# Optimization experiments

Hardware: AMD Instinct MI355X
Metric: run time of the kernel (lower is better)

Reference implementation:

```python
import jax, jax.numpy as jnp
import numpy as np

N_NODES = 50000
N_EDGES = 800000
D_NODE = 64
D_EDGE = 64


def setup_inputs() -> dict:
    key = jax.random.key(0)
    ks = jax.random.split(key, 8)
    s = lambda fan_in: 1.0 / np.sqrt(fan_in)
    return {
        "feats": jax.random.normal(ks[0], (N_NODES, D_NODE), dtype=jnp.float32),
        "edge_index": jax.random.randint(ks[1], (N_EDGES, 2), 0, N_NODES, dtype=jnp.int64),
        "edge_attr": jax.random.normal(ks[2], (N_EDGES, D_EDGE), dtype=jnp.float32),
        "W1e": jax.random.normal(ks[3], (2 * D_NODE + D_EDGE, 64), dtype=jnp.float32) * s(192),
        "b1e": jnp.zeros((64,), dtype=jnp.float32),
        "W2e": jax.random.normal(ks[4], (64, D_EDGE), dtype=jnp.float32) * s(64),
        "b2e": jnp.zeros((D_EDGE,), dtype=jnp.float32),
        "W1n": jax.random.normal(ks[5], (D_NODE + D_EDGE, 64), dtype=jnp.float32) * s(128),
        "b1n": jnp.zeros((64,), dtype=jnp.float32),
        "W2n": jax.random.normal(ks[6], (64, D_NODE), dtype=jnp.float32) * s(64),
        "b2n": jnp.zeros((D_NODE,), dtype=jnp.float32),
    }


def reference(feats, edge_index, edge_attr, W1e, b1e, W2e, b2e, W1n, b1n, W2n, b2n):
    r = edge_index[:, 0]
    c = edge_index[:, 1]
    n_nodes = feats.shape[0]

    # Edge model: gather source/target node feats, concat with edge_attr, MLP.
    x = jnp.concatenate([feats[r], feats[c], edge_attr], axis=1)  # [E, 2*d_node+d_edge]
    e = jax.nn.relu(x @ W1e + b1e) @ W2e + b2e                    # [E, d_edge]

    # Node model: mean-aggregate incoming edge messages by target node, concat, MLP.
    agg = jax.ops.segment_sum(e, c, num_segments=n_nodes)         # [N, d_edge]
    deg = jax.ops.segment_sum(jnp.ones((e.shape[0], 1), e.dtype), c, num_segments=n_nodes)
    agg = agg / jnp.maximum(deg, 1.0)
    h = jnp.concatenate([feats, agg], axis=1)                     # [N, d_node+d_edge]
    feats_out = jax.nn.relu(h @ W1n + b1n) @ W2n + b2n            # [N, d_node]

    return feats_out, e
```

## Files before the change

### kernel.cpp

```cpp
#include <hip/hip_runtime.h>

#define NN 50000
#define NE 800000
#define D 64

typedef float v4f __attribute__((ext_vector_type(4)));
typedef int v2i __attribute__((ext_vector_type(2)));

template <bool NT>
__device__ __forceinline__ void mlp_accum64(const float* __restrict__ x,
                                            const float* __restrict__ W,
                                            float scale, float* h) {
    const v4f* x4 = (const v4f*)x;
    #pragma unroll 1
    for (int k0 = 0; k0 < D; k0 += 8) {
        v4f v0, v1;
        if (NT) {
            v0 = __builtin_nontemporal_load(x4 + k0 / 4);
            v1 = __builtin_nontemporal_load(x4 + k0 / 4 + 1);
        } else {
            v0 = x4[k0 / 4];
            v1 = x4[k0 / 4 + 1];
        }
        float xa[8];
        xa[0] = v0[0]; xa[1] = v0[1]; xa[2] = v0[2]; xa[3] = v0[3];
        xa[4] = v1[0]; xa[5] = v1[1]; xa[6] = v1[2]; xa[7] = v1[3];
        #pragma unroll
        for (int kk = 0; kk < 8; ++kk) {
            const float xk = xa[kk] * scale;
            const float* Wr = W + (k0 + kk) * D;
            #pragma unroll
            for (int j = 0; j < D; ++j) h[j] = fmaf(xk, Wr[j], h[j]);
        }
    }
}

__device__ __forceinline__ void mlp_layer2(const float* __restrict__ W2,
                                           const float* __restrict__ b2,
                                           const float* h, float* acc,
                                           float* myrow) {
    #pragma unroll
    for (int j = 0; j < D; ++j) acc[j] = b2[j];
    #pragma unroll
    for (int half = 0; half < 2; ++half) {
        #pragma unroll
        for (int k = 0; k < 32; ++k) myrow[k] = fmaxf(h[half * 32 + k], 0.f);
        #pragma unroll 1
        for (int k = 0; k < 32; ++k) {
            const float hk = myrow[k];
            const float* Wr = W2 + (half * 32 + k) * D;
            #pragma unroll
            for (int j = 0; j < D; ++j) acc[j] = fmaf(hk, Wr[j], acc[j]);
        }
    }
}

__global__ __launch_bounds__(256) void edge_kernel(
    const float* __restrict__ feats, const int* __restrict__ ei,
    const float* __restrict__ ea, const float* __restrict__ W1,
    const float* __restrict__ b1, const float* __restrict__ W2,
    const float* __restrict__ b2, float* __restrict__ e_out,
    float* __restrict__ agg, float* __restrict__ deg) {
    __shared__ float tbuf[4][64 * 17];
    __shared__ int cbuf[4][64];
    const int tid = threadIdx.x;
    const int w = tid >> 6;
    const int lane = tid & 63;
    const int eid = blockIdx.x * 256 + tid;
    const int ebase = blockIdx.x * 256 + w * 64;

    const v2i rc = __builtin_nontemporal_load((const v2i*)ei + eid);
    const int r = rc[0];
    const int c = rc[1];
    cbuf[w][lane] = c;

    float h[D];
    #pragma unroll
    for (int j = 0; j < D; ++j) h[j] = b1[j];

    const float* xr = feats + (size_t)r * D;
    const float* xc = feats + (size_t)c * D;
    const float* xe = ea + (size_t)eid * D;

    #pragma unroll 1
    for (int s = 0; s < 2; ++s)
        mlp_accum64<false>((s == 0) ? xr : xc, W1 + s * D * D, 1.0f, h);
    mlp_accum64<true>(xe, W1 + 2 * D * D, 1.0f, h);

    #pragma unroll
    for (int k = 0; k < D; ++k) h[k] = fmaxf(h[k], 0.f);

    float* T = tbuf[w];
    const int es = lane >> 4;
    const int js = lane & 15;
    #pragma unroll 1
    for (int c0 = 0; c0 < D; c0 += 16) {
        #pragma unroll 1
        for (int jj = 0; jj < 16; ++jj) {
            const int j = c0 + jj;
            const float* Wc = W2 + j;
            float p0 = b2[j], p1 = 0.f, p2 = 0.f, p3 = 0.f;
            #pragma unroll
            for (int k = 0; k < D; k += 4) {
                p0 = fmaf(h[k + 0], Wc[(k + 0) * D], p0);
                p1 = fmaf(h[k + 1], Wc[(k + 1) * D], p1);
                p2 = fmaf(h[k + 2], Wc[(k + 2) * D], p2);
                p3 = fmaf(h[k + 3], Wc[(k + 3) * D], p3);
            }
            T[lane * 17 + jj] = (p0 + p1) + (p2 + p3);
        }
        #pragma unroll 1
        for (int g = 0; g < 16; ++g) {
            const int o = g * 4 + es;
            const float v = T[o * 17 + js];
            const int cd = cbuf[w][o];
            __builtin_nontemporal_store(
                v, e_out + (size_t)(ebase + o) * D + c0 + js);
            unsafeAtomicAdd(agg + (size_t)cd * D + c0 + js, v);
        }
    }
    unsafeAtomicAdd(deg + c, 1.0f);
}

__global__ __launch_bounds__(64) void node_kernel(
    const float* __restrict__ feats, const float* __restrict__ agg,
    const float* __restrict__ deg, const float* __restrict__ W1,
    const float* __restrict__ b1, const float* __restrict__ W2,
    const float* __restrict__ b2, float* __restrict__ out) {
    __shared__ float sh[64 * 33];
    const int tid = threadIdx.x;
    const int n = blockIdx.x * 64 + tid;
    if (n >= NN) return;

    float h[D];
    #pragma unroll
    for (int j = 0; j < D; ++j) h[j] = b1[j];

    const float rd = 1.0f / fmaxf(deg[n], 1.0f);

    mlp_accum64<false>(feats + (size_t)n * D, W1, 1.0f, h);
    mlp_accum64<false>(agg + (size_t)n * D, W1 + D * D, rd, h);

    float acc[D];
    mlp_layer2(W2, b2, h, acc, sh + tid * 33);

    float4* o4 = (float4*)(out + (size_t)n * D);
    #pragma unroll
    for (int q = 0; q < 16; ++q)
        o4[q] = make_float4(acc[4 * q + 0], acc[4 * q + 1],
                            acc[4 * q + 2], acc[4 * q + 3]);
}

extern "C" void kernel_launch(void* const* d_in, const int* in_sizes, int n_in,
                              void* d_out, int out_size, void* d_ws,
                              size_t ws_size, hipStream_t stream) {
    const float* feats = (const float*)d_in[0];
    const int* ei      = (const int*)d_in[1];
    const float* ea    = (const float*)d_in[2];
    const float* W1e   = (const float*)d_in[3];
    const float* b1e   = (const float*)d_in[4];
    const float* W2e   = (const float*)d_in[5];
    const float* b2e   = (const float*)d_in[6];
    const float* W1n   = (const float*)d_in[7];
    const float* b1n   = (const float*)d_in[8];
    const float* W2n   = (const float*)d_in[9];
    const float* b2n   = (const float*)d_in[10];

    float* out_f = (float*)d_out;
    float* feats_out = out_f;
    float* e_out = out_f + (size_t)NN * D;

    float* agg = (float*)d_ws;
    float* deg = agg + (size_t)NN * D;

    hipMemsetAsync(d_ws, 0, ((size_t)NN * D + NN) * sizeof(float), stream);

    edge_kernel<<<NE / 256, 256, 0, stream>>>(feats, ei, ea, W1e, b1e, W2e,
                                              b2e, e_out, agg, deg);
    node_kernel<<<(NN + 63) / 64, 64, 0, stream>>>(feats, agg, deg, W1n, b1n,
                                                   W2n, b2n, feats_out);
}
```

Measured before the change: 855.6 us.

## Prefetch edge inputs, restructure layer-2 loops, vectorize stores, split node MLP across 4 waves

The edge kernel's first layer becomes one 24-chunk loop that software-prefetches the next 8 input floats while computing the current chunk. Its second layer now accumulates 16 outputs at once, reading W2 rows instead of columns. e_out is written with 128-bit nontemporal stores, separate from the per-float atomic adds. The node kernel uses 256 threads per 64 nodes: each wave computes a 16-column slice, and the hidden layer is shared through LDS with a block barrier. This raises node-kernel parallelism and cuts per-thread register pressure, at the cost of redundant input loads and a sync.

```diff
diff --git a/kernel.cpp b/kernel.cpp
--- a/kernel.cpp
+++ b/kernel.cpp
@@ -6,54 +6,6 @@
 
 typedef float v4f __attribute__((ext_vector_type(4)));
 typedef int v2i __attribute__((ext_vector_type(2)));
-
-template <bool NT>
-__device__ __forceinline__ void mlp_accum64(const float* __restrict__ x,
-                                            const float* __restrict__ W,
-                                            float scale, float* h) {
-    const v4f* x4 = (const v4f*)x;
-    #pragma unroll 1
-    for (int k0 = 0; k0 < D; k0 += 8) {
-        v4f v0, v1;
-        if (NT) {
-            v0 = __builtin_nontemporal_load(x4 + k0 / 4);
-            v1 = __builtin_nontemporal_load(x4 + k0 / 4 + 1);
-        } else {
-            v0 = x4[k0 / 4];
-            v1 = x4[k0 / 4 + 1];
-        }
-        float xa[8];
-        xa[0] = v0[0]; xa[1] = v0[1]; xa[2] = v0[2]; xa[3] = v0[3];
-        xa[4] = v1[0]; xa[5] = v1[1]; xa[6] = v1[2]; xa[7] = v1[3];
-        #pragma unroll
-        for (int kk = 0; kk < 8; ++kk) {
-            const float xk = xa[kk] * scale;
-            const float* Wr = W + (k0 + kk) * D;
-            #pragma unroll
-            for (int j = 0; j < D; ++j) h[j] = fmaf(xk, Wr[j], h[j]);
-        }
-    }
-}
-
-__device__ __forceinline__ void mlp_layer2(const float* __restrict__ W2,
-                                           const float* __restrict__ b2,
-                                           const float* h, float* acc,
-                                           float* myrow) {
-    #pragma unroll
-    for (int j = 0; j < D; ++j) acc[j] = b2[j];
-    #pragma unroll
-    for (int half = 0; half < 2; ++half) {
-        #pragma unroll
-        for (int k = 0; k < 32; ++k) myrow[k] = fmaxf(h[half * 32 + k], 0.f);
-        #pragma unroll 1
-        for (int k = 0; k < 32; ++k) {
-            const float hk = myrow[k];
-            const float* Wr = W2 + (half * 32 + k) * D;
-            #pragma unroll
-            for (int j = 0; j < D; ++j) acc[j] = fmaf(hk, Wr[j], acc[j]);
-        }
-    }
-}
 
 __global__ __launch_bounds__(256) void edge_kernel(
     const float* __restrict__ feats, const int* __restrict__ ei,
@@ -78,14 +30,36 @@
     #pragma unroll
     for (int j = 0; j < D; ++j) h[j] = b1[j];
 
-    const float* xr = feats + (size_t)r * D;
-    const float* xc = feats + (size_t)c * D;
-    const float* xe = ea + (size_t)eid * D;
-
+    const v4f* s0 = (const v4f*)(feats + (size_t)r * D);
+    const v4f* s1 = (const v4f*)(feats + (size_t)c * D);
+    const v4f* s2 = (const v4f*)(ea + (size_t)eid * D);
+
+    v4f c0v = s0[0], c1v = s0[1];
     #pragma unroll 1
-    for (int s = 0; s < 2; ++s)
-        mlp_accum64<false>((s == 0) ? xr : xc, W1 + s * D * D, 1.0f, h);
-    mlp_accum64<true>(xe, W1 + 2 * D * D, 1.0f, h);
+    for (int cc = 0; cc < 24; ++cc) {
+        const int nc = cc + 1;
+        const v4f* nb = (nc < 8) ? s0 : ((nc < 16) ? s1 : s2);
+        const int off = (nc & 7) * 2;
+        v4f n0, n1;
+        if (nc >= 16) {
+            n0 = __builtin_nontemporal_load(nb + off);
+            n1 = __builtin_nontemporal_load(nb + off + 1);
+        } else {
+            n0 = nb[off];
+            n1 = nb[off + 1];
+        }
+        float xa[8] = {c0v[0], c0v[1], c0v[2], c0v[3],
+                       c1v[0], c1v[1], c1v[2], c1v[3]};
+        const float* Wr = W1 + cc * 8 * D;
+        #pragma unroll
+        for (int kk = 0; kk < 8; ++kk) {
+            const float xk = xa[kk];
+            #pragma unroll
+            for (int j = 0; j < D; ++j) h[j] = fmaf(xk, Wr[kk * D + j], h[j]);
+        }
+        c0v = n0;
+        c1v = n1;
+    }
 
     #pragma unroll
     for (int k = 0; k < D; ++k) h[k] = fmaxf(h[k], 0.f);
@@ -93,62 +67,111 @@
     float* T = tbuf[w];
     const int es = lane >> 4;
     const int js = lane & 15;
+    const int e4 = lane >> 2;
+    const int qd = lane & 3;
     #pragma unroll 1
     for (int c0 = 0; c0 < D; c0 += 16) {
+        float acc[16];
+        #pragma unroll
+        for (int j = 0; j < 16; ++j) acc[j] = b2[c0 + j];
+        #pragma unroll
+        for (int k = 0; k < D; ++k) {
+            const float hk = h[k];
+            const float* Wr = W2 + k * D + c0;
+            #pragma unroll
+            for (int j = 0; j < 16; ++j) acc[j] = fmaf(hk, Wr[j], acc[j]);
+        }
+        #pragma unroll
+        for (int i = 0; i < 16; ++i) T[lane * 17 + i] = acc[i];
         #pragma unroll 1
-        for (int jj = 0; jj < 16; ++jj) {
-            const int j = c0 + jj;
-            const float* Wc = W2 + j;
-            float p0 = b2[j], p1 = 0.f, p2 = 0.f, p3 = 0.f;
-            #pragma unroll
-            for (int k = 0; k < D; k += 4) {
-                p0 = fmaf(h[k + 0], Wc[(k + 0) * D], p0);
-                p1 = fmaf(h[k + 1], Wc[(k + 1) * D], p1);
-                p2 = fmaf(h[k + 2], Wc[(k + 2) * D], p2);
-                p3 = fmaf(h[k + 3], Wc[(k + 3) * D], p3);
-            }
-            T[lane * 17 + jj] = (p0 + p1) + (p2 + p3);
+        for (int g2 = 0; g2 < 4; ++g2) {
+            const int o = g2 * 16 + e4;
+            v4f v;
+            #pragma unroll
+            for (int i = 0; i < 4; ++i) v[i] = T[o * 17 + qd * 4 + i];
+            __builtin_nontemporal_store(
+                v, (v4f*)(e_out + (size_t)(ebase + o) * D + c0 + qd * 4));
         }
         #pragma unroll 1
         for (int g = 0; g < 16; ++g) {
             const int o = g * 4 + es;
             const float v = T[o * 17 + js];
             const int cd = cbuf[w][o];
-            __builtin_nontemporal_store(
-                v, e_out + (size_t)(ebase + o) * D + c0 + js);
             unsafeAtomicAdd(agg + (size_t)cd * D + c0 + js, v);
         }
     }
     unsafeAtomicAdd(deg + c, 1.0f);
 }
 
-__global__ __launch_bounds__(64) void node_kernel(
+__global__ __launch_bounds__(256) void node_kernel(
     const float* __restrict__ feats, const float* __restrict__ agg,
     const float* __restrict__ deg, const float* __restrict__ W1,
     const float* __restrict__ b1, const float* __restrict__ W2,
     const float* __restrict__ b2, float* __restrict__ out) {
-    __shared__ float sh[64 * 33];
+    __shared__ float sh[64 * 65];
     const int tid = threadIdx.x;
-    const int n = blockIdx.x * 64 + tid;
-    if (n >= NN) return;
-
-    float h[D];
-    #pragma unroll
-    for (int j = 0; j < D; ++j) h[j] = b1[j];
+    const int lane = tid & 63;
+    const int q = tid >> 6;
+    int n = blockIdx.x * 64 + lane;
+    const bool valid = (n < NN);
+    if (!valid) n = NN - 1;
 
     const float rd = 1.0f / fmaxf(deg[n], 1.0f);
 
-    mlp_accum64<false>(feats + (size_t)n * D, W1, 1.0f, h);
-    mlp_accum64<false>(agg + (size_t)n * D, W1 + D * D, rd, h);
-
-    float acc[D];
-    mlp_layer2(W2, b2, h, acc, sh + tid * 33);
-
-    float4* o4 = (float4*)(out + (size_t)n * D);
-    #pragma unroll
-    for (int q = 0; q < 16; ++q)
-        o4[q] = make_float4(acc[4 * q + 0], acc[4 * q + 1],
-                            acc[4 * q + 2], acc[4 * q + 3]);
+    float h16[16];
+    #pragma unroll
+    for (int j = 0; j < 16; ++j) h16[j] = b1[q * 16 + j];
+
+    const v4f* s0 = (const v4f*)(feats + (size_t)n * D);
+    const v4f* s1 = (const v4f*)(agg + (size_t)n * D);
+
+    v4f c0v = s0[0], c1v = s0[1];
+    #pragma unroll 1
+    for (int cc = 0; cc < 16; ++cc) {
+        const int nc = cc + 1;
+        const v4f* nb = (nc < 8) ? s0 : s1;
+        const int off = (nc & 7) * 2;
+        v4f n0 = nb[off], n1 = nb[off + 1];
+        const float sc = (cc < 8) ? 1.0f : rd;
+        float xa[8] = {c0v[0], c0v[1], c0v[2], c0v[3],
+                       c1v[0], c1v[1], c1v[2], c1v[3]};
+        const float* Wr = W1 + cc * 8 * D + q * 16;
+        #pragma unroll
+        for (int kk = 0; kk < 8; ++kk) {
+            const float xk = xa[kk] * sc;
+            #pragma unroll
+            for (int j = 0; j < 16; ++j)
+                h16[j] = fmaf(xk, Wr[kk * D + j], h16[j]);
+        }
+        c0v = n0;
+        c1v = n1;
+    }
+
+    #pragma unroll
+    for (int j = 0; j < 16; ++j)
+        sh[lane * 65 + q * 16 + j] = fmaxf(h16[j], 0.f);
+    __syncthreads();
+
+    float acc[16];
+    #pragma unroll
+    for (int j = 0; j < 16; ++j) acc[j] = b2[q * 16 + j];
+    #pragma unroll
+    for (int k = 0; k < D; ++k) {
+        const float hk = sh[lane * 65 + k];
+        const float* Wr = W2 + k * D + q * 16;
+        #pragma unroll
+        for (int j = 0; j < 16; ++j) acc[j] = fmaf(hk, Wr[j], acc[j]);
+    }
+
+    if (valid) {
+        v4f* o4 = (v4f*)(out + (size_t)n * D + q * 16);
+        #pragma unroll
+        for (int qq = 0; qq < 4; ++qq) {
+            v4f v = {acc[4 * qq + 0], acc[4 * qq + 1],
+                     acc[4 * qq + 2], acc[4 * qq + 3]};
+            o4[qq] = v;
+        }
+    }
 }
 
 extern "C" void kernel_launch(void* const* d_in, const int* in_sizes, int n_in,
@@ -177,6 +200,6 @@
 
     edge_kernel<<<NE / 256, 256, 0, stream>>>(feats, ei, ea, W1e, b1e, W2e,
                                               b2e, e_out, agg, deg);
-    node_kernel<<<(NN + 63) / 64, 64, 0, stream>>>(feats, agg, deg, W1n, b1n,
-                                                   W2n, b2n, feats_out);
+    node_kernel<<<(NN + 63) / 64, 256, 0, stream>>>(feats, agg, deg, W1n, b1n,
+                                                    W2n, b2n, feats_out);
 }
```

New measurement: 888.2 us. +3.8%, slower.
